# Optimization experiments

Hardware: AMD Instinct MI355X
Metric: run time of the kernel (lower is better)

## Reference

```python
import jax, jax.numpy as jnp
import numpy as np

EPS = 1e-12

def _l2norm(v):
    return v / (jnp.linalg.norm(v) + EPS)

def _spectral_norm_weight(W, u):
    # torch spectral_norm with n_power_iterations=1: v = norm(W^T u); u' = norm(W v);
    # sigma = u'^T W v with u', v detached; returns W / sigma.
    v = jax.lax.stop_gradient(_l2norm(W.T @ u))
    u2 = jax.lax.stop_gradient(_l2norm(W @ v))
    sigma = u2 @ (W @ v)
    return W / sigma

def setup_inputs() -> dict:
    key = jax.random.key(0)
    ks = jax.random.split(key, 8)
    C, H, W = 64, 96, 96
    Cfg = C // 8
    g = 1e-2  # small weight scale (module uses orthogonal init with tiny gain)
    return {
        "x":  jax.random.normal(ks[0], (1, C, H, W), jnp.float32),
        "Wf": jax.random.normal(ks[1], (Cfg, C), jnp.float32) * g,
        "bf": jnp.zeros((Cfg,), jnp.float32),
        "Wg": jax.random.normal(ks[2], (Cfg, C), jnp.float32) * g,
        "bg": jnp.zeros((Cfg,), jnp.float32),
        "Wh": jax.random.normal(ks[3], (C, C), jnp.float32) * g,
        "bh": jnp.zeros((C,), jnp.float32),
        "gamma": jax.random.normal(ks[4], (1,), jnp.float32),
        "uf": jax.random.normal(ks[5], (Cfg,), jnp.float32),
        "ug": jax.random.normal(ks[6], (Cfg,), jnp.float32),
        "uh": jax.random.normal(ks[7], (C,), jnp.float32),
    }

def reference(x, Wf, bf, Wg, bg, Wh, bh, gamma, uf, ug, uh):
    B, C, H, Wd = x.shape
    N = H * Wd
    xf = x.reshape(B, C, N)  # 1x1 convs act per-pixel -> matmul over channel dim
    Wf_sn = _spectral_norm_weight(Wf, uf)
    Wg_sn = _spectral_norm_weight(Wg, ug)
    Wh_sn = _spectral_norm_weight(Wh, uh)
    f_flat = jnp.einsum('oc,bcn->bon', Wf_sn, xf) + bf[:, None]  # [B,Cfg,N]
    g_flat = jnp.einsum('oc,bcn->bon', Wg_sn, xf) + bg[:, None]  # [B,Cfg,N]
    h_flat = jnp.einsum('oc,bcn->bon', Wh_sn, xf) + bh[:, None]  # [B,C,N]
    # s[b,n,m] = sum_k g[b,k,n] * f[b,k,m]  (g^T f)
    s = jnp.einsum('bkn,bkm->bnm', g_flat, f_flat)  # [B,N,N]
    beta = jax.nn.softmax(s, axis=1)                # softmax over dim=1 (g axis)
    o = jnp.einsum('bcn,bnm->bcm', h_flat, beta)    # [B,C,N]
    o = o.reshape(B, C, H, Wd)
    return gamma * o + x
```

## Files before the change

kernel.cpp:

```cpp
#include <hip/hip_runtime.h>
#include <hip/hip_bf16.h>

#define NPIX 9216
#define SPLIT 8
#define NSEG (NPIX / SPLIT)
#define NT (NSEG / 32)
#define MTILES (NPIX / 16)

typedef __attribute__((ext_vector_type(4))) float f32x4;
typedef __attribute__((ext_vector_type(8))) short bf16x8;
typedef __attribute__((ext_vector_type(2))) unsigned int u32x2;

__device__ __forceinline__ void gload_lds16(const void* g, void* l) {
  __builtin_amdgcn_global_load_lds(
      (const __attribute__((address_space(1))) unsigned int*)g,
      (__attribute__((address_space(3))) unsigned int*)l, 16, 0, 0);
}
__device__ __forceinline__ void gload_lds4(const void* g, void* l) {
  __builtin_amdgcn_global_load_lds(
      (const __attribute__((address_space(1))) unsigned int*)g,
      (__attribute__((address_space(3))) unsigned int*)l, 4, 0, 0);
}
#define LDS_OFF(p) ((unsigned)(unsigned long long)(const __attribute__((address_space(3))) char*)(const char*)(p))

__global__ __launch_bounds__(256) void fgh_kernel(
    const float* __restrict__ x,
    const float* __restrict__ Wf, const float* __restrict__ bfv,
    const float* __restrict__ Wg, const float* __restrict__ bgv,
    const float* __restrict__ Wh, const float* __restrict__ bhv,
    const float* __restrict__ uf, const float* __restrict__ ug,
    const float* __restrict__ uh,
    ushort* __restrict__ Qp, ushort* __restrict__ Kp, ushort* __restrict__ Vt2) {
  __shared__ float vsh[64];
  __shared__ float is_s[3];
  const int tid = threadIdx.x;
  if (tid < 64) {
    const int t = tid;
    for (int widx = 0; widx < 3; ++widx) {
      const float* W = (widx == 0) ? Wf : (widx == 1) ? Wg : Wh;
      const float* u = (widx == 0) ? uf : (widx == 1) ? ug : uh;
      const int O = (widx == 2) ? 64 : 8;
      float v = 0.f;
      for (int o = 0; o < O; ++o) v += W[o * 64 + t] * u[o];
      float s = v * v;
      for (int off = 32; off; off >>= 1) s += __shfl_xor(s, off);
      vsh[t] = v / (sqrtf(s) + 1e-12f);
      float wv = 0.f;
      if (t < O) { for (int c = 0; c < 64; ++c) wv += W[t * 64 + c] * vsh[c]; }
      float s2 = (t < O) ? wv * wv : 0.f;
      for (int off = 32; off; off >>= 1) s2 += __shfl_xor(s2, off);
      const float nw = sqrtf(s2);
      if (t == 0) is_s[widx] = (nw + 1e-12f) / s2;
    }
  }
  __syncthreads();

  const int p = blockIdx.x * 256 + tid;
  const int by = blockIdx.y;
  float xv[64];
  #pragma unroll
  for (int c = 0; c < 64; ++c) xv[c] = x[c * NPIX + p];

  if (by == 0) {
    const float isf = is_s[0], isg = is_s[1];
    for (int r = 0; r < 8; ++r) {
      float a = 0.f;
      #pragma unroll
      for (int c = 0; c < 64; ++c) a += Wf[r * 64 + c] * xv[c];
      const float vq = (a * isf + bfv[r]) * 0.25f;
      const __hip_bfloat16 h = __float2bfloat16(vq);
      const float hf = __bfloat162float(h);
      const __hip_bfloat16 lo = __float2bfloat16(vq - hf);
      Qp[p * 16 + r]     = *(const ushort*)&h;
      Qp[p * 16 + 8 + r] = *(const ushort*)&lo;
    }
    for (int r = 0; r < 8; ++r) {
      float a = 0.f;
      #pragma unroll
      for (int c = 0; c < 64; ++c) a += Wg[r * 64 + c] * xv[c];
      const float val = a * isg + bgv[r];
      const __hip_bfloat16 h = __float2bfloat16(val);
      const float hf = __bfloat162float(h);
      const __hip_bfloat16 lo = __float2bfloat16(val - hf);
      Kp[p * 16 + r]     = *(const ushort*)&h;
      Kp[p * 16 + 8 + r] = *(const ushort*)&lo;
    }
  } else {
    const float ish = is_s[2];
    const int tile = p >> 5;
    const int nr = p & 31;
    const int tt = nr >> 4, gg = (nr >> 2) & 3, ii = nr & 3;
    ushort* vout = Vt2 + (size_t)tile * 2048 + gg * 8 + tt * 4 + ii;
    const int rbase = (by - 1) * 16;
    for (int rr = 0; rr < 16; ++rr) {
      const int r = rbase + rr;
      float a = 0.f;
      #pragma unroll
      for (int c = 0; c < 64; ++c) a += Wh[r * 64 + c] * xv[c];
      const float val = a * ish + bhv[r];
      const __hip_bfloat16 hv = __float2bfloat16(val);
      vout[r * 32] = *(const ushort*)&hv;
    }
  }
}

__global__ __launch_bounds__(256) void attn_kernel(
    const ushort* __restrict__ Qp, const ushort* __restrict__ Kp,
    const ushort* __restrict__ Vt2,
    ushort* __restrict__ Om,
    float* __restrict__ Sm) {
  __shared__ ushort Vs[4][2048];
  __shared__ ushort Ks[4][512];
  const int tid  = threadIdx.x;
  const int w    = tid >> 6;
  const int l    = tid & 63;
  const int mloc = l & 15;
  const int g    = l >> 4;
  const int spl  = blockIdx.y;
  const int mrow = blockIdx.x * 64 + w * 16 + mloc;

  bf16x8 qh = *(const bf16x8*)(Qp + mrow * 16);
  bf16x8 ql = *(const bf16x8*)(Qp + mrow * 16 + 8);
  asm volatile("" : "+v"(qh), "+v"(ql));

  const int n0 = spl * NSEG;
  const char* vsrc = (const char*)Vt2 + ((size_t)(n0 >> 5)) * 4096 + w * 1024 + l * 16;
  const char* ksrc = (const char*)Kp + (size_t)n0 * 32 + w * 256 + l * 4;

  #define STAGE(t_) do {                                                  \
    const int b_ = (t_) & 3;                                              \
    gload_lds16(vsrc + (size_t)(t_) * 4096, (char*)&Vs[b_][0] + w * 1024);\
    gload_lds4 (ksrc + (size_t)(t_) * 1024, (char*)&Ks[b_][0] + w * 256); \
  } while (0)

  STAGE(0);
  STAGE(1);

  const unsigned ks_base = LDS_OFF(&Ks[0][0]);
  const unsigned vs_base = LDS_OFF(&Vs[0][0]);

  float mx = -INFINITY, ls = 0.f;
  const f32x4 zero = {0.f, 0.f, 0.f, 0.f};
  f32x4 acc0 = zero, acc1 = zero, acc2 = zero, acc3 = zero;

  for (int t = 0; t < NT; ++t) {
    const int b = t & 3;
    if (t + 2 < NT) {
      STAGE(t + 2);
      asm volatile("s_waitcnt vmcnt(4)" ::: "memory");
    } else if (t + 1 < NT) {
      asm volatile("s_waitcnt vmcnt(2)" ::: "memory");
    } else {
      asm volatile("s_waitcnt vmcnt(0)" ::: "memory");
    }
    __builtin_amdgcn_s_barrier();

    const unsigned kaddr = ks_base + b * 1024 + mloc * 32;
    const unsigned vaddr = vs_base + b * 4096 + mloc * 64 + g * 16;
    bf16x8 kh0, kl0, kh1, kl1, v0, v1, v2, v3;
    asm volatile("ds_read_b128 %0, %1"            : "=v"(kh0) : "v"(kaddr));
    asm volatile("ds_read_b128 %0, %1 offset:16"  : "=v"(kl0) : "v"(kaddr));
    asm volatile("ds_read_b128 %0, %1 offset:512" : "=v"(kh1) : "v"(kaddr));
    asm volatile("ds_read_b128 %0, %1 offset:528" : "=v"(kl1) : "v"(kaddr));
    asm volatile("ds_read_b128 %0, %1"            : "=v"(v0)  : "v"(vaddr));
    asm volatile("ds_read_b128 %0, %1 offset:1024": "=v"(v1)  : "v"(vaddr));
    asm volatile("ds_read_b128 %0, %1 offset:2048": "=v"(v2)  : "v"(vaddr));
    asm volatile("ds_read_b128 %0, %1 offset:3072": "=v"(v3)  : "v"(vaddr));
    asm volatile("s_waitcnt lgkmcnt(0)" ::: "memory");
    __builtin_amdgcn_sched_barrier(0);

    f32x4 s0 = zero, s1 = zero;
    s0 = __builtin_amdgcn_mfma_f32_16x16x32_bf16(kh0, qh, s0, 0, 0, 0);
    s1 = __builtin_amdgcn_mfma_f32_16x16x32_bf16(kh1, qh, s1, 0, 0, 0);
    s0 = __builtin_amdgcn_mfma_f32_16x16x32_bf16(kh0, ql, s0, 0, 0, 0);
    s1 = __builtin_amdgcn_mfma_f32_16x16x32_bf16(kh1, ql, s1, 0, 0, 0);
    s0 = __builtin_amdgcn_mfma_f32_16x16x32_bf16(kl0, qh, s0, 0, 0, 0);
    s1 = __builtin_amdgcn_mfma_f32_16x16x32_bf16(kl1, qh, s1, 0, 0, 0);

    const float tm = fmaxf(
        fmaxf(fmaxf(s0[0], s0[1]), fmaxf(s0[2], s0[3])),
        fmaxf(fmaxf(s1[0], s1[1]), fmaxf(s1[2], s1[3])));
    if (__any(tm > mx + 8.0f)) {
      float tr = fmaxf(tm, __shfl_xor(tm, 16));
      tr = fmaxf(tr, __shfl_xor(tr, 32));
      const float mxn = fmaxf(mx, tr);
      const float corr = __expf(mx - mxn);
      ls *= corr;
      const float c0 = __shfl(corr, (g << 2) + 0);
      const float c1 = __shfl(corr, (g << 2) + 1);
      const float c2 = __shfl(corr, (g << 2) + 2);
      const float c3 = __shfl(corr, (g << 2) + 3);
      acc0[0] *= c0; acc0[1] *= c1; acc0[2] *= c2; acc0[3] *= c3;
      acc1[0] *= c0; acc1[1] *= c1; acc1[2] *= c2; acc1[3] *= c3;
      acc2[0] *= c0; acc2[1] *= c1; acc2[2] *= c2; acc2[3] *= c3;
      acc3[0] *= c0; acc3[1] *= c1; acc3[2] *= c2; acc3[3] *= c3;
      mx = mxn;
    }
    float pj[8];
    pj[0] = __expf(s0[0] - mx); pj[1] = __expf(s0[1] - mx);
    pj[2] = __expf(s0[2] - mx); pj[3] = __expf(s0[3] - mx);
    pj[4] = __expf(s1[0] - mx); pj[5] = __expf(s1[1] - mx);
    pj[6] = __expf(s1[2] - mx); pj[7] = __expf(s1[3] - mx);
    ls += ((pj[0] + pj[1]) + (pj[2] + pj[3])) + ((pj[4] + pj[5]) + (pj[6] + pj[7]));

    union { unsigned int u[4]; bf16x8 v; } pu;
    #pragma unroll
    for (int jj = 0; jj < 4; ++jj) {
      unsigned int r;
      asm("v_cvt_pk_bf16_f32 %0, %1, %2" : "=v"(r) : "v"(pj[2 * jj]), "v"(pj[2 * jj + 1]));
      pu.u[jj] = r;
    }
    acc0 = __builtin_amdgcn_mfma_f32_16x16x32_bf16(pu.v, v0, acc0, 0, 0, 0);
    acc1 = __builtin_amdgcn_mfma_f32_16x16x32_bf16(pu.v, v1, acc1, 0, 0, 0);
    acc2 = __builtin_amdgcn_mfma_f32_16x16x32_bf16(pu.v, v2, acc2, 0, 0, 0);
    acc3 = __builtin_amdgcn_mfma_f32_16x16x32_bf16(pu.v, v3, acc3, 0, 0, 0);
  }
  #undef STAGE

  ls += __shfl_xor(ls, 16);
  ls += __shfl_xor(ls, 32);

  const size_t mt = (size_t)blockIdx.x * 4 + w;
  ushort* Ob = Om + (mt * SPLIT + spl) * 1024;
  float*  Sb = Sm + (mt * SPLIT + spl) * 32;
  #pragma unroll
  for (int ct = 0; ct < 4; ++ct) {
    const f32x4 a = (ct == 0) ? acc0 : (ct == 1) ? acc1 : (ct == 2) ? acc2 : acc3;
    unsigned int r0, r1;
    asm("v_cvt_pk_bf16_f32 %0, %1, %2" : "=v"(r0) : "v"(a[0]), "v"(a[1]));
    asm("v_cvt_pk_bf16_f32 %0, %1, %2" : "=v"(r1) : "v"(a[2]), "v"(a[3]));
    u32x2 pk; pk[0] = r0; pk[1] = r1;
    *(u32x2*)(Ob + (ct * 16 + mloc) * 16 + 4 * g) = pk;
  }
  if (l < 16) { Sb[l] = mx; Sb[16 + l] = ls; }
}

__global__ __launch_bounds__(256) void combine_kernel(
    const ushort* __restrict__ Om, const float* __restrict__ Sm,
    const float* __restrict__ x, const float* __restrict__ gammap,
    float* __restrict__ out) {
  const int mt = blockIdx.x;
  const int m0 = mt * 16;
  const float gamma = gammap[0];
  const float* Sb = Sm + (size_t)mt * SPLIT * 32;
  const ushort* Ob = Om + (size_t)mt * SPLIT * 1024;
  for (int e = threadIdx.x; e < 1024; e += 256) {
    const int m = e & 15, c = e >> 4;
    float M = -INFINITY;
    #pragma unroll
    for (int s = 0; s < SPLIT; ++s) M = fmaxf(M, Sb[s * 32 + m]);
    float L = 0.f, val = 0.f;
    #pragma unroll
    for (int s = 0; s < SPLIT; ++s) {
      const float wgt = __expf(Sb[s * 32 + m] - M);
      L += Sb[s * 32 + 16 + m] * wgt;
      union { unsigned int i; float f; } cv;
      cv.i = ((unsigned int)Ob[s * 1024 + e]) << 16;
      val += cv.f * wgt;
    }
    const int idx = c * NPIX + m0 + m;
    out[idx] = gamma * (val / L) + x[idx];
  }
}

extern "C" void kernel_launch(void* const* d_in, const int* in_sizes, int n_in,
                              void* d_out, int out_size, void* d_ws, size_t ws_size,
                              hipStream_t stream) {
  const float* x     = (const float*)d_in[0];
  const float* Wf    = (const float*)d_in[1];
  const float* bf    = (const float*)d_in[2];
  const float* Wg    = (const float*)d_in[3];
  const float* bg    = (const float*)d_in[4];
  const float* Wh    = (const float*)d_in[5];
  const float* bh    = (const float*)d_in[6];
  const float* gamma = (const float*)d_in[7];
  const float* uf    = (const float*)d_in[8];
  const float* ug    = (const float*)d_in[9];
  const float* uh    = (const float*)d_in[10];
  float* out = (float*)d_out;

  char* ws = (char*)d_ws;
  ushort* Qp  = (ushort*)(ws + 256);
  ushort* Kp  = (ushort*)(ws + 256 + NPIX * 16 * 2);
  ushort* Vt2 = (ushort*)(ws + 256 + 2 * NPIX * 16 * 2);
  size_t off = 256 + (size_t)2 * NPIX * 16 * 2 + (size_t)NPIX * 64 * 2;
  ushort* Om = (ushort*)(ws + off);
  float*  Sm = (float*)(ws + off + (size_t)MTILES * SPLIT * 1024 * 2);

  fgh_kernel<<<dim3(NPIX / 256, 5), 256, 0, stream>>>(x, Wf, bf, Wg, bg, Wh, bh,
                                                      uf, ug, uh, Qp, Kp, Vt2);
  attn_kernel<<<dim3(NPIX / 64, SPLIT), 256, 0, stream>>>(Qp, Kp, Vt2, Om, Sm);
  combine_kernel<<<MTILES, 256, 0, stream>>>(Om, Sm, x, gamma, out);
}
```

Baseline: 83.55 us.

## Restructure projection kernel, swizzle V/K layouts, and raise split-K to 16

The f/g/h projection kernel now stages a 16-pixel x tile and all weights in LDS. Each thread computes five output rows, so x is read once instead of five times across blockIdx.y. K is stored tile-major so the hi/lo halves sit in separate 256-byte rows, and V is XOR-swizzled, both to cut LDS bank conflicts in the attention loop. The attention split is templated and raised to 16 when the workspace is large enough, trading more partials and combine work for more parallel blocks.

```diff
diff --git a/kernel.cpp b/kernel.cpp
--- a/kernel.cpp
+++ b/kernel.cpp
@@ -2,9 +2,6 @@
 #include <hip/hip_bf16.h>
 
 #define NPIX 9216
-#define SPLIT 8
-#define NSEG (NPIX / SPLIT)
-#define NT (NSEG / 32)
 #define MTILES (NPIX / 16)
 
 typedef __attribute__((ext_vector_type(4))) float f32x4;
@@ -31,9 +28,22 @@
     const float* __restrict__ uf, const float* __restrict__ ug,
     const float* __restrict__ uh,
     ushort* __restrict__ Qp, ushort* __restrict__ Kp, ushort* __restrict__ Vt2) {
+  __shared__ float xs[64][16];
+  __shared__ float Ws[80][65];
   __shared__ float vsh[64];
   __shared__ float is_s[3];
   const int tid = threadIdx.x;
+
+  const int p0 = blockIdx.x * 16;
+  #pragma unroll
+  for (int e = tid; e < 1024; e += 256) {
+    const int c = e >> 4, px = e & 15;
+    xs[c][px] = x[c * NPIX + p0 + px];
+  }
+  for (int e = tid; e < 512; e += 256) Ws[e >> 6][e & 63]       = Wf[e];
+  for (int e = tid; e < 512; e += 256) Ws[8 + (e >> 6)][e & 63]  = Wg[e];
+  for (int e = tid; e < 4096; e += 256) Ws[16 + (e >> 6)][e & 63] = Wh[e];
+
   if (tid < 64) {
     const int t = tid;
     for (int widx = 0; widx < 3; ++widx) {
@@ -55,60 +65,56 @@
   }
   __syncthreads();
 
-  const int p = blockIdx.x * 256 + tid;
-  const int by = blockIdx.y;
-  float xv[64];
+  const int px = tid & 15;
+  const int rg = tid >> 4;
+  const int p  = p0 + px;
+  float acc[5] = {0.f, 0.f, 0.f, 0.f, 0.f};
+  for (int c = 0; c < 64; ++c) {
+    const float xv = xs[c][px];
+    #pragma unroll
+    for (int j = 0; j < 5; ++j) acc[j] += Ws[rg * 5 + j][c] * xv;
+  }
+
+  const int tile = p >> 5, nt = p & 31;
+  const int tt = nt >> 4, gg = (nt >> 2) & 3, ii = nt & 3;
+  const int kbase = tile * 512 + nt * 8;
   #pragma unroll
-  for (int c = 0; c < 64; ++c) xv[c] = x[c * NPIX + p];
-
-  if (by == 0) {
-    const float isf = is_s[0], isg = is_s[1];
-    for (int r = 0; r < 8; ++r) {
-      float a = 0.f;
-      #pragma unroll
-      for (int c = 0; c < 64; ++c) a += Wf[r * 64 + c] * xv[c];
-      const float vq = (a * isf + bfv[r]) * 0.25f;
+  for (int j = 0; j < 5; ++j) {
+    const int r = rg * 5 + j;
+    if (r < 8) {
+      const float vq = (acc[j] * is_s[0] + bfv[r]) * 0.25f;
       const __hip_bfloat16 h = __float2bfloat16(vq);
       const float hf = __bfloat162float(h);
       const __hip_bfloat16 lo = __float2bfloat16(vq - hf);
       Qp[p * 16 + r]     = *(const ushort*)&h;
       Qp[p * 16 + 8 + r] = *(const ushort*)&lo;
-    }
-    for (int r = 0; r < 8; ++r) {
-      float a = 0.f;
-      #pragma unroll
-      for (int c = 0; c < 64; ++c) a += Wg[r * 64 + c] * xv[c];
-      const float val = a * isg + bgv[r];
+    } else if (r < 16) {
+      const int rk = r - 8;
+      const float val = acc[j] * is_s[1] + bgv[rk];
       const __hip_bfloat16 h = __float2bfloat16(val);
       const float hf = __bfloat162float(h);
       const __hip_bfloat16 lo = __float2bfloat16(val - hf);
-      Kp[p * 16 + r]     = *(const ushort*)&h;
-      Kp[p * 16 + 8 + r] = *(const ushort*)&lo;
-    }
-  } else {
-    const float ish = is_s[2];
-    const int tile = p >> 5;
-    const int nr = p & 31;
-    const int tt = nr >> 4, gg = (nr >> 2) & 3, ii = nr & 3;
-    ushort* vout = Vt2 + (size_t)tile * 2048 + gg * 8 + tt * 4 + ii;
-    const int rbase = (by - 1) * 16;
-    for (int rr = 0; rr < 16; ++rr) {
-      const int r = rbase + rr;
-      float a = 0.f;
-      #pragma unroll
-      for (int c = 0; c < 64; ++c) a += Wh[r * 64 + c] * xv[c];
-      const float val = a * ish + bhv[r];
+      Kp[kbase + rk]        = *(const ushort*)&h;
+      Kp[kbase + 256 + rk]  = *(const ushort*)&lo;
+    } else {
+      const int rv = r - 16;
+      const float val = acc[j] * is_s[2] + bhv[rv];
       const __hip_bfloat16 hv = __float2bfloat16(val);
-      vout[r * 32] = *(const ushort*)&hv;
-    }
-  }
-}
-
+      const int idx = tile * 2048 +
+          ((rv * 32 + gg * 8 + tt * 4 + ii) ^ (((rv >> 1) & 7) << 3));
+      Vt2[idx] = *(const ushort*)&hv;
+    }
+  }
+}
+
+template <int S>
 __global__ __launch_bounds__(256) void attn_kernel(
     const ushort* __restrict__ Qp, const ushort* __restrict__ Kp,
     const ushort* __restrict__ Vt2,
     ushort* __restrict__ Om,
     float* __restrict__ Sm) {
+  constexpr int NSEG = NPIX / S;
+  constexpr int NT = NSEG / 32;
   __shared__ ushort Vs[4][2048];
   __shared__ ushort Ks[4][512];
   const int tid  = threadIdx.x;
@@ -125,7 +131,7 @@
 
   const int n0 = spl * NSEG;
   const char* vsrc = (const char*)Vt2 + ((size_t)(n0 >> 5)) * 4096 + w * 1024 + l * 16;
-  const char* ksrc = (const char*)Kp + (size_t)n0 * 32 + w * 256 + l * 4;
+  const char* ksrc = (const char*)Kp + ((size_t)(n0 >> 5)) * 1024 + w * 256 + l * 4;
 
   #define STAGE(t_) do {                                                  \
     const int b_ = (t_) & 3;                                              \
@@ -138,6 +144,7 @@
 
   const unsigned ks_base = LDS_OFF(&Ks[0][0]);
   const unsigned vs_base = LDS_OFF(&Vs[0][0]);
+  const unsigned vswz = (mloc * 64 + g * 16) ^ (((mloc >> 1) & 7) << 4);
 
   float mx = -INFINITY, ls = 0.f;
   const f32x4 zero = {0.f, 0.f, 0.f, 0.f};
@@ -155,13 +162,13 @@
     }
     __builtin_amdgcn_s_barrier();
 
-    const unsigned kaddr = ks_base + b * 1024 + mloc * 32;
-    const unsigned vaddr = vs_base + b * 4096 + mloc * 64 + g * 16;
+    const unsigned kaddr = ks_base + b * 1024 + mloc * 16;
+    const unsigned vaddr = vs_base + b * 4096 + vswz;
     bf16x8 kh0, kl0, kh1, kl1, v0, v1, v2, v3;
     asm volatile("ds_read_b128 %0, %1"            : "=v"(kh0) : "v"(kaddr));
-    asm volatile("ds_read_b128 %0, %1 offset:16"  : "=v"(kl0) : "v"(kaddr));
-    asm volatile("ds_read_b128 %0, %1 offset:512" : "=v"(kh1) : "v"(kaddr));
-    asm volatile("ds_read_b128 %0, %1 offset:528" : "=v"(kl1) : "v"(kaddr));
+    asm volatile("ds_read_b128 %0, %1 offset:256" : "=v"(kh1) : "v"(kaddr));
+    asm volatile("ds_read_b128 %0, %1 offset:512" : "=v"(kl0) : "v"(kaddr));
+    asm volatile("ds_read_b128 %0, %1 offset:768" : "=v"(kl1) : "v"(kaddr));
     asm volatile("ds_read_b128 %0, %1"            : "=v"(v0)  : "v"(vaddr));
     asm volatile("ds_read_b128 %0, %1 offset:1024": "=v"(v1)  : "v"(vaddr));
     asm volatile("ds_read_b128 %0, %1 offset:2048": "=v"(v2)  : "v"(vaddr));
@@ -221,8 +228,8 @@
   ls += __shfl_xor(ls, 32);
 
   const size_t mt = (size_t)blockIdx.x * 4 + w;
-  ushort* Ob = Om + (mt * SPLIT + spl) * 1024;
-  float*  Sb = Sm + (mt * SPLIT + spl) * 32;
+  ushort* Ob = Om + (mt * S + spl) * 1024;
+  float*  Sb = Sm + (mt * S + spl) * 32;
   #pragma unroll
   for (int ct = 0; ct < 4; ++ct) {
     const f32x4 a = (ct == 0) ? acc0 : (ct == 1) ? acc1 : (ct == 2) ? acc2 : acc3;
@@ -235,6 +242,7 @@
   if (l < 16) { Sb[l] = mx; Sb[16 + l] = ls; }
 }
 
+template <int S>
 __global__ __launch_bounds__(256) void combine_kernel(
     const ushort* __restrict__ Om, const float* __restrict__ Sm,
     const float* __restrict__ x, const float* __restrict__ gammap,
@@ -242,16 +250,16 @@
   const int mt = blockIdx.x;
   const int m0 = mt * 16;
   const float gamma = gammap[0];
-  const float* Sb = Sm + (size_t)mt * SPLIT * 32;
-  const ushort* Ob = Om + (size_t)mt * SPLIT * 1024;
+  const float* Sb = Sm + (size_t)mt * S * 32;
+  const ushort* Ob = Om + (size_t)mt * S * 1024;
   for (int e = threadIdx.x; e < 1024; e += 256) {
     const int m = e & 15, c = e >> 4;
     float M = -INFINITY;
     #pragma unroll
-    for (int s = 0; s < SPLIT; ++s) M = fmaxf(M, Sb[s * 32 + m]);
+    for (int s = 0; s < S; ++s) M = fmaxf(M, Sb[s * 32 + m]);
     float L = 0.f, val = 0.f;
     #pragma unroll
-    for (int s = 0; s < SPLIT; ++s) {
+    for (int s = 0; s < S; ++s) {
       const float wgt = __expf(Sb[s * 32 + m] - M);
       L += Sb[s * 32 + 16 + m] * wgt;
       union { unsigned int i; float f; } cv;
@@ -283,12 +291,19 @@
   ushort* Qp  = (ushort*)(ws + 256);
   ushort* Kp  = (ushort*)(ws + 256 + NPIX * 16 * 2);
   ushort* Vt2 = (ushort*)(ws + 256 + 2 * NPIX * 16 * 2);
-  size_t off = 256 + (size_t)2 * NPIX * 16 * 2 + (size_t)NPIX * 64 * 2;
+  const size_t off = 256 + (size_t)2 * NPIX * 16 * 2 + (size_t)NPIX * 64 * 2;
   ushort* Om = (ushort*)(ws + off);
-  float*  Sm = (float*)(ws + off + (size_t)MTILES * SPLIT * 1024 * 2);
-
-  fgh_kernel<<<dim3(NPIX / 256, 5), 256, 0, stream>>>(x, Wf, bf, Wg, bg, Wh, bh,
-                                                      uf, ug, uh, Qp, Kp, Vt2);
-  attn_kernel<<<dim3(NPIX / 64, SPLIT), 256, 0, stream>>>(Qp, Kp, Vt2, Om, Sm);
-  combine_kernel<<<MTILES, 256, 0, stream>>>(Om, Sm, x, gamma, out);
-}
+  const size_t need16 = off + (size_t)MTILES * 16 * 1024 * 2 + (size_t)MTILES * 16 * 32 * 4;
+
+  fgh_kernel<<<NPIX / 16, 256, 0, stream>>>(x, Wf, bf, Wg, bg, Wh, bh,
+                                            uf, ug, uh, Qp, Kp, Vt2);
+  if (ws_size >= need16) {
+    float* Sm = (float*)(ws + off + (size_t)MTILES * 16 * 1024 * 2);
+    attn_kernel<16><<<dim3(NPIX / 64, 16), 256, 0, stream>>>(Qp, Kp, Vt2, Om, Sm);
+    combine_kernel<16><<<MTILES, 256, 0, stream>>>(Om, Sm, x, gamma, out);
+  } else {
+    float* Sm = (float*)(ws + off + (size_t)MTILES * 8 * 1024 * 2);
+    attn_kernel<8><<<dim3(NPIX / 64, 8), 256, 0, stream>>>(Qp, Kp, Vt2, Om, Sm);
+    combine_kernel<8><<<MTILES, 256, 0, stream>>>(Om, Sm, x, gamma, out);
+  }
+}
```

After: 90.80 us. 1.09x slower.
